# Kernel tuning notes

Measured on AMD Instinct MI355X. Metric: run time of the kernel, lower is better.

## Reference

```python
import jax, jax.numpy as jnp
import numpy as np

D = 2048      # d_hidden
F = 1408      # d_expert (routed)
E = 8         # n_routed_experts
K = 2         # n_experts_per_token
FS = 2816     # shared expert width = d_expert * n_shared_experts
B, S = 2, 1024


def setup_inputs() -> dict:
    key = jax.random.key(0)
    ks = jax.random.split(key, 9)
    sc = 0.02
    return {
        "x": jax.random.normal(ks[0], (B, S, D), dtype=jnp.float32),
        "Wr": jax.random.normal(ks[1], (E, D), dtype=jnp.float32) * sc,   # router Linear(d_hidden, E).weight
        "Wg": jax.random.normal(ks[2], (E, F, D), dtype=jnp.float32) * sc,  # per-expert W_gate.weight [F,D]
        "Wu": jax.random.normal(ks[3], (E, F, D), dtype=jnp.float32) * sc,  # per-expert W_up.weight
        "Wd": jax.random.normal(ks[4], (E, D, F), dtype=jnp.float32) * sc,  # per-expert W_down.weight [D,F]
        "Wsg": jax.random.normal(ks[5], (FS, D), dtype=jnp.float32) * sc,   # shared expert W_gate
        "Wsu": jax.random.normal(ks[6], (FS, D), dtype=jnp.float32) * sc,   # shared expert W_up
        "Wsd": jax.random.normal(ks[7], (D, FS), dtype=jnp.float32) * sc,   # shared expert W_down
    }


def reference(x, Wr, Wg, Wu, Wd, Wsg, Wsu, Wsd):
    silu = jax.nn.silu

    # Shared expert: SwiGLU FFN over all tokens
    sg = silu(jnp.einsum("bsd,fd->bsf", x, Wsg))
    su = jnp.einsum("bsd,fd->bsf", x, Wsu)
    shared_out = jnp.einsum("bsf,df->bsd", sg * su, Wsd)

    # Gating: softmax over expert logits, then top-k (sum-combine is order-invariant)
    logits = jnp.einsum("bsd,ed->bse", x, Wr)
    scores = jax.nn.softmax(logits, axis=-1)
    topk_scores, topk_idx = jax.lax.top_k(scores, K)            # [B,S,K]
    # Dense combine weights [B,S,E]: topk score where selected, else 0
    w_full = jnp.sum(jax.nn.one_hot(topk_idx, E, dtype=x.dtype) * topk_scores[..., None], axis=-2)

    # Routed experts (dense-over-experts equivalent of sorted grouped-GEMM dispatch)
    g = silu(jnp.einsum("bsd,efd->bsef", x, Wg))                # [B,S,E,F]
    u = jnp.einsum("bsd,efd->bsef", x, Wu)
    out_e = jnp.einsum("bsef,edf->bsed", g * u, Wd)             # [B,S,E,D]
    routed_out = jnp.einsum("bsed,bse->bsd", out_e, w_full)

    return routed_out + shared_out
```

## Files before the change

### kernel.cpp

```cpp
#include <hip/hip_runtime.h>
#include <hip/hip_bf16.h>

#define D_HID 2048
#define F_EXP 1408
#define E_NUM 8
#define FS_SH 2816
#define T_TOK 2048

#define O_WSG 0
#define O_WSU 5767168
#define O_WG  11534336
#define O_WU  34603008
#define O_WSD 57671680
#define O_WD  63438848
#define W_TOT 86507520

#define MAXT 24
#define GU_SH_BLK 176
#define GU_GEMM   440
#define GU_CONV   64
#define DN_GRID   512
#define DN_SH_BLK 128
#define RT_BLK    512
#define WC_BLK    1408

typedef __attribute__((ext_vector_type(8))) short bf16x8;
typedef __attribute__((ext_vector_type(4))) float f32x4;
typedef __attribute__((ext_vector_type(4))) unsigned short u16x4;

#define AS1 __attribute__((address_space(1)))
#define AS3 __attribute__((address_space(3)))

__device__ __forceinline__ unsigned short f2bf(float f){
  unsigned u = __float_as_uint(f);
  u += 0x7fffu + ((u >> 16) & 1u);
  return (unsigned short)(u >> 16);
}

__global__ __launch_bounds__(256) void prep_kernel(
    const float* __restrict__ x,  const float* __restrict__ Wr,
    const float* __restrict__ Wsg, const float* __restrict__ Wsu,
    const float* __restrict__ Wg,  const float* __restrict__ Wu,
    unsigned short* __restrict__ xb, unsigned short* __restrict__ wb,
    int* __restrict__ topk_e, float* __restrict__ topk_w)
{
  const int b = blockIdx.x;
  if (b >= RT_BLK){
    const int cb = b - RT_BLK;
    const long nchunk = (long)O_WSD / 8;
    for (long i = (long)cb*256 + threadIdx.x; i < nchunk; i += (long)WC_BLK*256){
      const long e0 = i * 8;
      const float* src; long lo;
      if      (e0 < (long)O_WSU){ src = Wsg; lo = e0; }
      else if (e0 < (long)O_WG ){ src = Wsu; lo = e0 - O_WSU; }
      else if (e0 < (long)O_WU ){ src = Wg;  lo = e0 - O_WG;  }
      else                      { src = Wu;  lo = e0 - O_WU;  }
      const float4 va = ((const float4*)(src + lo))[0];
      const float4 vb = ((const float4*)(src + lo))[1];
      u16x4 h0, h1;
      h0[0]=f2bf(va.x); h0[1]=f2bf(va.y); h0[2]=f2bf(va.z); h0[3]=f2bf(va.w);
      h1[0]=f2bf(vb.x); h1[1]=f2bf(vb.y); h1[2]=f2bf(vb.z); h1[3]=f2bf(vb.w);
      ((u16x4*)(wb + e0))[0] = h0;
      ((u16x4*)(wb + e0))[1] = h1;
    }
    return;
  }
  const int lane = threadIdx.x & 63;
  const int t = b*4 + (threadIdx.x >> 6);
  const float* xt = x + (size_t)t * D_HID;
  unsigned short* xbt = xb + (size_t)t * D_HID;
  float acc[E_NUM];
  #pragma unroll
  for (int e=0;e<E_NUM;e++) acc[e]=0.f;
  #pragma unroll
  for (int j=0;j<8;j++){
    const int d = j*256 + lane*4;
    const float4 v = *(const float4*)(xt + d);
    u16x4 h;
    h[0]=f2bf(v.x); h[1]=f2bf(v.y); h[2]=f2bf(v.z); h[3]=f2bf(v.w);
    *(u16x4*)(xbt + d) = h;
    #pragma unroll
    for (int e=0;e<E_NUM;e++){
      const float4 w = *(const float4*)(Wr + e*D_HID + d);
      acc[e] += v.x*w.x + v.y*w.y + v.z*w.z + v.w*w.w;
    }
  }
  #pragma unroll
  for (int e=0;e<E_NUM;e++){
    #pragma unroll
    for (int off=32; off>0; off>>=1) acc[e] += __shfl_xor(acc[e], off);
  }
  if (lane==0){
    float m = acc[0];
    #pragma unroll
    for (int e=1;e<E_NUM;e++) m = fmaxf(m, acc[e]);
    float p[E_NUM]; float s = 0.f;
    #pragma unroll
    for (int e=0;e<E_NUM;e++){ p[e] = expf(acc[e]-m); s += p[e]; }
    const float inv = 1.f/s;
    int i0=0; float b0=p[0];
    #pragma unroll
    for (int e=1;e<E_NUM;e++) if (p[e] > b0){ b0=p[e]; i0=e; }
    int i1=-1; float b1=-1.f;
    #pragma unroll
    for (int e=0;e<E_NUM;e++) if (e!=i0 && p[e] > b1){ b1=p[e]; i1=e; }
    topk_e[t*2+0]=i0; topk_e[t*2+1]=i1;
    topk_w[t*2+0]=b0*inv; topk_w[t*2+1]=b1*inv;
  }
}

__global__ __launch_bounds__(1024) void build_lists_kernel(
    const int* __restrict__ topk_e, const float* __restrict__ topk_w,
    int* __restrict__ cnt, int* __restrict__ offs,
    int* __restrict__ assign_token, float* __restrict__ assign_w,
    int* __restrict__ token_slot,
    int* __restrict__ tile_rowbase, int* __restrict__ tile_e,
    int* __restrict__ tile_valid, int* __restrict__ n_rt)
{
  const int tid  = threadIdx.x;
  const int lane = tid & 63;
  const int wv   = tid >> 6;
  __shared__ int wsum[E_NUM][16];
  __shared__ int tot_s[E_NUM];
  __shared__ int offs_s[E_NUM];

  int   e_loc[4];
  float w_loc[4];
  #pragma unroll
  for (int j=0;j<4;j++){ e_loc[j]=topk_e[tid*4+j]; w_loc[j]=topk_w[tid*4+j]; }

  int c[E_NUM];
  #pragma unroll
  for (int e=0;e<E_NUM;e++){
    int s = 0;
    #pragma unroll
    for (int j=0;j<4;j++) s += (e_loc[j]==e) ? 1 : 0;
    c[e] = s;
  }
  int pre[E_NUM];
  #pragma unroll
  for (int e=0;e<E_NUM;e++){
    int v = c[e];
    #pragma unroll
    for (int off=1; off<64; off<<=1){
      int t = __shfl_up(v, off);
      if (lane >= off) v += t;
    }
    if (lane==63) wsum[e][wv] = v;
    pre[e] = v - c[e];
  }
  __syncthreads();
  if (tid < E_NUM){
    int s = 0;
    #pragma unroll
    for (int w=0; w<16; w++){ int t = wsum[tid][w]; wsum[tid][w] = s; s += t; }
    tot_s[tid] = s;
    cnt[tid]   = s;
  }
  __syncthreads();
  if (tid == 0){
    int s = 0;
    #pragma unroll
    for (int e=0;e<E_NUM;e++){ offs_s[e] = s; offs[e] = s; s += tot_s[e]; }
    int ntl = 0;
    for (int e=0;e<E_NUM;e++){
      for (int r=0; r<tot_s[e]; r+=256){
        tile_rowbase[ntl] = offs_s[e] + r;
        tile_e[ntl]       = e;
        int v = tot_s[e] - r; if (v > 256) v = 256;
        tile_valid[ntl]   = v;
        ntl++;
      }
    }
    n_rt[0] = ntl;
    for (int i=ntl;i<MAXT;i++){ tile_rowbase[i]=0; tile_e[i]=0; tile_valid[i]=0; }
  }
  __syncthreads();
  int local[E_NUM];
  #pragma unroll
  for (int e=0;e<E_NUM;e++) local[e]=0;
  #pragma unroll
  for (int j=0;j<4;j++){
    const int e = e_loc[j];
    int pos = 0;
    #pragma unroll
    for (int ee=0; ee<E_NUM; ee++)
      if (e == ee) pos = offs_s[ee] + wsum[ee][wv] + pre[ee] + local[ee];
    #pragma unroll
    for (int ee=0; ee<E_NUM; ee++) local[ee] += (e == ee) ? 1 : 0;
    const int entry = tid*4 + j;
    assign_token[pos] = entry >> 1;
    assign_w[pos]     = w_loc[j];
    token_slot[entry] = pos;
  }
}

__global__ __launch_bounds__(512,1) void gateup_fused(
    const unsigned short* __restrict__ xb,
    unsigned short* __restrict__ wb,
    const float* __restrict__ Wsd_f, const float* __restrict__ Wd_f,
    unsigned short* __restrict__ h_shared,
    unsigned short* __restrict__ h_routed,
    const int* __restrict__ tile_rowbase, const int* __restrict__ tile_e,
    const int* __restrict__ tile_valid, const int* __restrict__ n_rt,
    const int* __restrict__ assign_token)
{
  __shared__ __align__(16) char As[4][256*64];
  __shared__ __align__(16) char Bg[4][128*64];
  __shared__ __align__(16) char Bu[4][128*64];

  const int tid  = threadIdx.x;
  const int braw = blockIdx.x;

  if (braw >= GU_GEMM){
    const int cb = braw - GU_GEMM;
    const long nchunk = (long)(W_TOT - O_WSD) / 8;
    for (long i = (long)cb*512 + tid; i < nchunk; i += (long)GU_CONV*512){
      const long e0 = (long)O_WSD + i * 8;
      const float* src; long lo;
      if (e0 < (long)O_WD){ src = Wsd_f; lo = e0 - O_WSD; } else { src = Wd_f; lo = e0 - O_WD; }
      const float4 va = ((const float4*)(src + lo))[0];
      const float4 vb = ((const float4*)(src + lo))[1];
      u16x4 h0, h1;
      h0[0]=f2bf(va.x); h0[1]=f2bf(va.y); h0[2]=f2bf(va.z); h0[3]=f2bf(va.w);
      h1[0]=f2bf(vb.x); h1[1]=f2bf(vb.y); h1[2]=f2bf(vb.z); h1[3]=f2bf(vb.w);
      ((u16x4*)(wb + e0))[0] = h0;
      ((u16x4*)(wb + e0))[1] = h1;
    }
    return;
  }

  const int b = (braw % 8) * (GU_GEMM/8) + braw / 8;

  const int lane = tid & 63;
  const int wave = tid >> 6;
  const int wr = wave >> 1;
  const int wc = wave & 1;

  int nt, rowbase, valid, gather;
  const unsigned short *wg_base, *wu_base;
  unsigned short* H; int N;
  if (b < GU_SH_BLK){
    nt = b >> 3; const int mtile = b & 7;
    rowbase = mtile*256; valid = 256; gather = 0;
    wg_base = wb + O_WSG + (size_t)(nt*128) * D_HID;
    wu_base = wb + O_WSU + (size_t)(nt*128) * D_HID;
    H = h_shared; N = FS_SH;
  } else {
    const int rb = b - GU_SH_BLK;
    const int tile = rb % MAXT;
    nt = rb / MAXT;
    if (tile >= n_rt[0]) return;
    rowbase = tile_rowbase[tile];
    valid   = tile_valid[tile];
    const int e = tile_e[tile];
    gather = 1;
    wg_base = wb + O_WG + ((size_t)e*F_EXP + nt*128) * D_HID;
    wu_base = wb + O_WU + ((size_t)e*F_EXP + nt*128) * D_HID;
    H = h_routed; N = F_EXP;
  }

  f32x4 accg[4][4], accu[4][4];
  const f32x4 z = {0.f,0.f,0.f,0.f};
  #pragma unroll
  for (int m=0;m<4;m++)
    #pragma unroll
    for (int n=0;n<4;n++){ accg[m][n]=z; accu[m][n]=z; }

  const char* asrc[2];
  const int rowmax = rowbase + valid - 1;
  #pragma unroll
  for (int p=0;p<2;p++){
    const int c = p*512 + tid;
    const int row = c >> 2, slot = c & 3;
    const int col16 = slot ^ ((row>>1)&3);
    int idx = rowbase + row;
    if (idx > rowmax) idx = rowmax;
    const size_t grow = gather ? (size_t)assign_token[idx] : (size_t)idx;
    asrc[p] = (const char*)(xb + grow * (size_t)D_HID) + (col16<<4);
  }
  const int brw = tid >> 2, bsl = tid & 3;
  const int bcol16 = bsl ^ ((brw>>1)&3);
  const char* gsrc = (const char*)(wg_base + (size_t)brw * D_HID) + (bcol16<<4);
  const char* usrc = (const char*)(wu_base + (size_t)brw * D_HID) + (bcol16<<4);

  auto stage = [&](int bi, int kt){
    #pragma unroll
    for (int p=0;p<2;p++)
      __builtin_amdgcn_global_load_lds(
        (const AS1 void*)(asrc[p] + kt*64),
        (AS3 void*)(&As[bi][(p*512 + tid)*16]), 16, 0, 0);
    __builtin_amdgcn_global_load_lds(
        (const AS1 void*)(gsrc + kt*64),
        (AS3 void*)(&Bg[bi][tid*16]), 16, 0, 0);
    __builtin_amdgcn_global_load_lds(
        (const AS1 void*)(usrc + kt*64),
        (AS3 void*)(&Bu[bi][tid*16]), 16, 0, 0);
  };

  const int nK = D_HID / 32;
  stage(0,0); stage(1,1); stage(2,2);

  const int arow0 = wr*64 + (lane & 15);
  const int brow0 = wc*64 + (lane & 15);
  const int sread = (lane >> 4) << 4;

  #pragma unroll 1
  for (int kt = 0; kt < nK; ++kt){
    if (kt < nK-2)       asm volatile("s_waitcnt vmcnt(8)\n\ts_barrier" ::: "memory");
    else if (kt == nK-2) asm volatile("s_waitcnt vmcnt(4)\n\ts_barrier" ::: "memory");
    else                 asm volatile("s_waitcnt vmcnt(0)\n\ts_barrier" ::: "memory");
    const int bi = kt & 3;
    bf16x8 a[4], bgr[4], bur[4];
    #pragma unroll
    for (int m=0;m<4;m++){
      const int r = arow0 + m*16;
      a[m] = *(const bf16x8*)(&As[bi][r*64 + (sread ^ (((r>>1)&3)<<4))]);
    }
    #pragma unroll
    for (int n=0;n<4;n++){
      const int r = brow0 + n*16;
      const int ofs = r*64 + (sread ^ (((r>>1)&3)<<4));
      bgr[n] = *(const bf16x8*)(&Bg[bi][ofs]);
      bur[n] = *(const bf16x8*)(&Bu[bi][ofs]);
    }
    if (kt + 3 < nK) stage((kt+3)&3, kt+3);
    #pragma unroll
    for (int m=0;m<4;m++)
      #pragma unroll
      for (int n=0;n<4;n++){
        accg[m][n] = __builtin_amdgcn_mfma_f32_16x16x32_bf16(a[m], bgr[n], accg[m][n], 0,0,0);
        accu[m][n] = __builtin_amdgcn_mfma_f32_16x16x32_bf16(a[m], bur[n], accu[m][n], 0,0,0);
      }
  }

  const int colbase = nt*128 + wc*64;
  #pragma unroll
  for (int m=0;m<4;m++){
    #pragma unroll
    for (int r=0;r<4;r++){
      const int rr = wr*64 + m*16 + ((lane >> 4) << 2) + r;
      if (rr < valid){
        unsigned short* orow = H + (size_t)(rowbase + rr) * N;
        #pragma unroll
        for (int n=0;n<4;n++){
          const int col = colbase + n*16 + (lane & 15);
          const float g = accg[m][n][r];
          const float u = accu[m][n][r];
          const float h = (g / (1.f + __expf(-g))) * u;
          orow[col] = f2bf(h);
        }
      }
    }
  }
}

__global__ __launch_bounds__(512,1) void down_fused(
    const unsigned short* __restrict__ h_shared,
    const unsigned short* __restrict__ h_routed,
    const unsigned short* __restrict__ wb,
    float* __restrict__ out, float* __restrict__ y_routed,
    const int* __restrict__ tile_rowbase, const int* __restrict__ tile_e,
    const int* __restrict__ tile_valid, const int* __restrict__ n_rt,
    const float* __restrict__ assign_w)
{
  __shared__ __align__(16) char As[4][256*64];
  __shared__ __align__(16) char Bs[4][128*64];

  const int tid  = threadIdx.x;
  const int braw = blockIdx.x;
  const int b = (braw % 8) * (DN_GRID/8) + braw / 8;
  const int lane = tid & 63;
  const int wave = tid >> 6;
  const int wr = wave >> 1, wc = wave & 1;

  int nt, rowbase, valid, weighted, K;
  const unsigned short *A, *w_base;
  float* Out;
  if (b < DN_SH_BLK){
    nt = b >> 3; const int mtile = b & 7;
    rowbase = mtile*256; valid = 256; weighted = 0;
    A = h_shared; K = FS_SH;
    w_base = wb + O_WSD + (size_t)(nt*128) * FS_SH;
    Out = out;
  } else {
    const int rb = b - DN_SH_BLK;
    const int tile = rb % MAXT;
    nt = rb / MAXT;
    if (tile >= n_rt[0]) return;
    rowbase = tile_rowbase[tile];
    valid   = tile_valid[tile];
    const int e = tile_e[tile];
    weighted = 1;
    A = h_routed; K = F_EXP;
    w_base = wb + O_WD + ((size_t)e*D_HID + nt*128) * F_EXP;
    Out = y_routed;
  }
  const size_t K2 = (size_t)K * 2;

  f32x4 acc[4][4];
  const f32x4 z = {0.f,0.f,0.f,0.f};
  #pragma unroll
  for (int m=0;m<4;m++)
    #pragma unroll
    for (int n=0;n<4;n++) acc[m][n]=z;

  const char* asrc[2];
  const int rowmax = rowbase + valid - 1;
  #pragma unroll
  for (int p=0;p<2;p++){
    const int c = p*512 + tid;
    const int row = c >> 2, slot = c & 3;
    const int col16 = slot ^ ((row>>1)&3);
    int idx = rowbase + row;
    if (idx > rowmax) idx = rowmax;
    asrc[p] = (const char*)A + (size_t)idx * K2 + (col16<<4);
  }
  const int brw = tid >> 2, bsl = tid & 3;
  const int bcol16 = bsl ^ ((brw>>1)&3);
  const char* bsrc = (const char*)w_base + (size_t)brw * K2 + (bcol16<<4);

  auto stage = [&](int bi, int kt){
    #pragma unroll
    for (int p=0;p<2;p++)
      __builtin_amdgcn_global_load_lds(
        (const AS1 void*)(asrc[p] + kt*64),
        (AS3 void*)(&As[bi][(p*512 + tid)*16]), 16, 0, 0);
    __builtin_amdgcn_global_load_lds(
        (const AS1 void*)(bsrc + kt*64),
        (AS3 void*)(&Bs[bi][tid*16]), 16, 0, 0);
  };

  const int nK = K / 32;
  stage(0,0); stage(1,1); stage(2,2);

  const int arow0 = wr*64 + (lane & 15);
  const int brow0 = wc*64 + (lane & 15);
  const int sread = (lane >> 4) << 4;

  #pragma unroll 1
  for (int kt = 0; kt < nK; ++kt){
    if (kt < nK-2)       asm volatile("s_waitcnt vmcnt(6)\n\ts_barrier" ::: "memory");
    else if (kt == nK-2) asm volatile("s_waitcnt vmcnt(3)\n\ts_barrier" ::: "memory");
    else                 asm volatile("s_waitcnt vmcnt(0)\n\ts_barrier" ::: "memory");
    const int bi = kt & 3;
    bf16x8 a[4], bb[4];
    #pragma unroll
    for (int m=0;m<4;m++){
      const int r = arow0 + m*16;
      a[m] = *(const bf16x8*)(&As[bi][r*64 + (sread ^ (((r>>1)&3)<<4))]);
    }
    #pragma unroll
    for (int n=0;n<4;n++){
      const int r = brow0 + n*16;
      bb[n] = *(const bf16x8*)(&Bs[bi][r*64 + (sread ^ (((r>>1)&3)<<4))]);
    }
    if (kt + 3 < nK) stage((kt+3)&3, kt+3);
    #pragma unroll
    for (int m=0;m<4;m++)
      #pragma unroll
      for (int n=0;n<4;n++)
        acc[m][n] = __builtin_amdgcn_mfma_f32_16x16x32_bf16(a[m], bb[n], acc[m][n], 0,0,0);
  }

  const int colbase = nt*128 + wc*64;
  #pragma unroll
  for (int m=0;m<4;m++){
    #pragma unroll
    for (int r=0;r<4;r++){
      const int rr = wr*64 + m*16 + ((lane >> 4) << 2) + r;
      if (rr < valid){
        float w = 1.f;
        if (weighted) w = assign_w[rowbase + rr];
        float* orow = Out + (size_t)(rowbase + rr) * D_HID;
        #pragma unroll
        for (int n=0;n<4;n++){
          const int col = colbase + n*16 + (lane & 15);
          orow[col] = acc[m][n][r] * w;
        }
      }
    }
  }
}

__global__ void combine_kernel(float* __restrict__ out, const float* __restrict__ y,
                               const int* __restrict__ token_slot){
  const int i  = blockIdx.x * blockDim.x + threadIdx.x;
  const int t  = i >> 9;
  const int r4 = i & 511;
  const int s0 = token_slot[t*2+0];
  const int s1 = token_slot[t*2+1];
  const float4 a = ((const float4*)(y + (size_t)s0 * D_HID))[r4];
  const float4 b = ((const float4*)(y + (size_t)s1 * D_HID))[r4];
  float4 o = ((float4*)out)[i];
  o.x += a.x + b.x; o.y += a.y + b.y; o.z += a.z + b.z; o.w += a.w + b.w;
  ((float4*)out)[i] = o;
}

extern "C" void kernel_launch(void* const* d_in, const int* in_sizes, int n_in,
                              void* d_out, int out_size, void* d_ws, size_t ws_size,
                              hipStream_t stream){
  const float* x   = (const float*)d_in[0];
  const float* Wr  = (const float*)d_in[1];
  const float* Wg  = (const float*)d_in[2];
  const float* Wu  = (const float*)d_in[3];
  const float* Wd  = (const float*)d_in[4];
  const float* Wsg = (const float*)d_in[5];
  const float* Wsu = (const float*)d_in[6];
  const float* Wsd = (const float*)d_in[7];
  float* out = (float*)d_out;
  (void)in_sizes; (void)n_in; (void)out_size; (void)ws_size;

  char* ws = (char*)d_ws;
  size_t off = 0;
  auto alloc = [&](size_t bytes)->char*{
    char* p = ws + off; off += (bytes + 255) & ~(size_t)255; return p;
  };

  unsigned short* wb       = (unsigned short*)alloc((size_t)W_TOT * 2);
  unsigned short* xb       = (unsigned short*)alloc((size_t)T_TOK * D_HID * 2);
  unsigned short* h_shared = (unsigned short*)alloc((size_t)T_TOK * FS_SH * 2);
  unsigned short* h_routed = (unsigned short*)alloc((size_t)T_TOK * 2 * F_EXP * 2);
  float*          y_routed = (float*)alloc((size_t)T_TOK * 2 * D_HID * 4);
  int*   topk_e       = (int*)alloc(T_TOK*2*sizeof(int));
  float* topk_w       = (float*)alloc(T_TOK*2*sizeof(float));
  int*   cnt          = (int*)alloc(E_NUM*sizeof(int));
  int*   offs         = (int*)alloc(E_NUM*sizeof(int));
  int*   assign_token = (int*)alloc(T_TOK*2*sizeof(int));
  float* assign_w     = (float*)alloc(T_TOK*2*sizeof(float));
  int*   token_slot   = (int*)alloc(T_TOK*2*sizeof(int));
  int*   tile_rowbase = (int*)alloc(MAXT*sizeof(int));
  int*   tile_e       = (int*)alloc(MAXT*sizeof(int));
  int*   tile_valid   = (int*)alloc(MAXT*sizeof(int));
  int*   n_rt         = (int*)alloc(sizeof(int));

  prep_kernel<<<RT_BLK + WC_BLK, 256, 0, stream>>>(
      x, Wr, Wsg, Wsu, Wg, Wu, xb, wb, topk_e, topk_w);
  build_lists_kernel<<<1, 1024, 0, stream>>>(topk_e, topk_w, cnt, offs,
      assign_token, assign_w, token_slot, tile_rowbase, tile_e, tile_valid, n_rt);

  gateup_fused<<<GU_GEMM + GU_CONV, 512, 0, stream>>>(
      xb, wb, Wsd, Wd, h_shared, h_routed, tile_rowbase, tile_e, tile_valid, n_rt, assign_token);
  down_fused<<<DN_GRID, 512, 0, stream>>>(
      h_shared, h_routed, wb, out, y_routed, tile_rowbase, tile_e, tile_valid, n_rt, assign_w);

  combine_kernel<<<(T_TOK*D_HID/4)/256, 256, 0, stream>>>(out, y_routed, token_slot);
}
```

Before: 371.9 us.

## Double-buffer LDS fragment reads in registers and raise MFMA wave priority

Both GEMM main loops are restructured so the A/B fragments for step kt+1 are read from LDS into a second register set while step kt's MFMAs run. The gate/up MFMAs are split into two passes, and MFMA sections are wrapped in s_setprio with one combined waitcnt and barrier per step. This aims to hide LDS read latency behind matrix math. Launch bounds also change to 2 blocks per CU. That caps registers and, given the large LDS footprint, may not raise occupancy and could cause spills.

```diff
diff --git a/kernel.cpp b/kernel.cpp
--- a/kernel.cpp
+++ b/kernel.cpp
@@ -195,7 +195,7 @@
   }
 }
 
-__global__ __launch_bounds__(512,1) void gateup_fused(
+__global__ __launch_bounds__(512,2) void gateup_fused(
     const unsigned short* __restrict__ xb,
     unsigned short* __restrict__ wb,
     const float* __restrict__ Wsd_f, const float* __restrict__ Wd_f,
@@ -298,20 +298,11 @@
         (AS3 void*)(&Bu[bi][tid*16]), 16, 0, 0);
   };
 
-  const int nK = D_HID / 32;
-  stage(0,0); stage(1,1); stage(2,2);
-
   const int arow0 = wr*64 + (lane & 15);
   const int brow0 = wc*64 + (lane & 15);
   const int sread = (lane >> 4) << 4;
 
-  #pragma unroll 1
-  for (int kt = 0; kt < nK; ++kt){
-    if (kt < nK-2)       asm volatile("s_waitcnt vmcnt(8)\n\ts_barrier" ::: "memory");
-    else if (kt == nK-2) asm volatile("s_waitcnt vmcnt(4)\n\ts_barrier" ::: "memory");
-    else                 asm volatile("s_waitcnt vmcnt(0)\n\ts_barrier" ::: "memory");
-    const int bi = kt & 3;
-    bf16x8 a[4], bgr[4], bur[4];
+  auto read_abg = [&](int bi, bf16x8* a, bf16x8* bg){
     #pragma unroll
     for (int m=0;m<4;m++){
       const int r = arow0 + m*16;
@@ -320,18 +311,51 @@
     #pragma unroll
     for (int n=0;n<4;n++){
       const int r = brow0 + n*16;
-      const int ofs = r*64 + (sread ^ (((r>>1)&3)<<4));
-      bgr[n] = *(const bf16x8*)(&Bg[bi][ofs]);
-      bur[n] = *(const bf16x8*)(&Bu[bi][ofs]);
+      bg[n] = *(const bf16x8*)(&Bg[bi][r*64 + (sread ^ (((r>>1)&3)<<4))]);
+    }
+  };
+
+  const int nK = D_HID / 32;
+  stage(0,0); stage(1,1); stage(2,2);
+  asm volatile("s_waitcnt vmcnt(8)\n\ts_barrier" ::: "memory");
+
+  bf16x8 aA[4], bgA[4], aB[4], bgB[4];
+  read_abg(0, aA, bgA);
+  asm volatile("s_waitcnt lgkmcnt(0) vmcnt(4)\n\ts_barrier" ::: "memory");
+
+  auto body = [&](int kt, bf16x8* aC, bf16x8* bgC, bf16x8* aN, bf16x8* bgN){
+    if (kt + 1 < nK) read_abg((kt+1)&3, aN, bgN);
+    bf16x8 bu[4];
+    {
+      const int bi = kt & 3;
+      #pragma unroll
+      for (int n=0;n<4;n++){
+        const int r = brow0 + n*16;
+        bu[n] = *(const bf16x8*)(&Bu[bi][r*64 + (sread ^ (((r>>1)&3)<<4))]);
+      }
     }
     if (kt + 3 < nK) stage((kt+3)&3, kt+3);
+    __builtin_amdgcn_s_setprio(1);
     #pragma unroll
     for (int m=0;m<4;m++)
       #pragma unroll
-      for (int n=0;n<4;n++){
-        accg[m][n] = __builtin_amdgcn_mfma_f32_16x16x32_bf16(a[m], bgr[n], accg[m][n], 0,0,0);
-        accu[m][n] = __builtin_amdgcn_mfma_f32_16x16x32_bf16(a[m], bur[n], accu[m][n], 0,0,0);
-      }
+      for (int n=0;n<4;n++)
+        accg[m][n] = __builtin_amdgcn_mfma_f32_16x16x32_bf16(aC[m], bgC[n], accg[m][n], 0,0,0);
+    #pragma unroll
+    for (int m=0;m<4;m++)
+      #pragma unroll
+      for (int n=0;n<4;n++)
+        accu[m][n] = __builtin_amdgcn_mfma_f32_16x16x32_bf16(aC[m], bu[n], accu[m][n], 0,0,0);
+    __builtin_amdgcn_s_setprio(0);
+    if (kt + 3 < nK) asm volatile("s_waitcnt lgkmcnt(0) vmcnt(4)\n\ts_barrier" ::: "memory");
+    else             asm volatile("s_waitcnt lgkmcnt(0) vmcnt(0)\n\ts_barrier" ::: "memory");
+    __builtin_amdgcn_sched_barrier(0);
+  };
+
+  #pragma unroll 1
+  for (int kt = 0; kt < nK; kt += 2){
+    body(kt,   aA, bgA, aB, bgB);
+    body(kt+1, aB, bgB, aA, bgA);
   }
 
   const int colbase = nt*128 + wc*64;
@@ -355,7 +379,7 @@
   }
 }
 
-__global__ __launch_bounds__(512,1) void down_fused(
+__global__ __launch_bounds__(512,2) void down_fused(
     const unsigned short* __restrict__ h_shared,
     const unsigned short* __restrict__ h_routed,
     const unsigned short* __restrict__ wb,
@@ -431,20 +455,11 @@
         (AS3 void*)(&Bs[bi][tid*16]), 16, 0, 0);
   };
 
-  const int nK = K / 32;
-  stage(0,0); stage(1,1); stage(2,2);
-
   const int arow0 = wr*64 + (lane & 15);
   const int brow0 = wc*64 + (lane & 15);
   const int sread = (lane >> 4) << 4;
 
-  #pragma unroll 1
-  for (int kt = 0; kt < nK; ++kt){
-    if (kt < nK-2)       asm volatile("s_waitcnt vmcnt(6)\n\ts_barrier" ::: "memory");
-    else if (kt == nK-2) asm volatile("s_waitcnt vmcnt(3)\n\ts_barrier" ::: "memory");
-    else                 asm volatile("s_waitcnt vmcnt(0)\n\ts_barrier" ::: "memory");
-    const int bi = kt & 3;
-    bf16x8 a[4], bb[4];
+  auto read_ab = [&](int bi, bf16x8* a, bf16x8* bb){
     #pragma unroll
     for (int m=0;m<4;m++){
       const int r = arow0 + m*16;
@@ -455,12 +470,35 @@
       const int r = brow0 + n*16;
       bb[n] = *(const bf16x8*)(&Bs[bi][r*64 + (sread ^ (((r>>1)&3)<<4))]);
     }
+  };
+
+  const int nK = K / 32;
+  stage(0,0); stage(1,1); stage(2,2);
+  asm volatile("s_waitcnt vmcnt(6)\n\ts_barrier" ::: "memory");
+
+  bf16x8 aA[4], bbA[4], aB[4], bbB[4];
+  read_ab(0, aA, bbA);
+  asm volatile("s_waitcnt lgkmcnt(0) vmcnt(3)\n\ts_barrier" ::: "memory");
+
+  auto body = [&](int kt, bf16x8* aC, bf16x8* bC, bf16x8* aN, bf16x8* bN){
+    if (kt + 1 < nK) read_ab((kt+1)&3, aN, bN);
     if (kt + 3 < nK) stage((kt+3)&3, kt+3);
+    __builtin_amdgcn_s_setprio(1);
     #pragma unroll
     for (int m=0;m<4;m++)
       #pragma unroll
       for (int n=0;n<4;n++)
-        acc[m][n] = __builtin_amdgcn_mfma_f32_16x16x32_bf16(a[m], bb[n], acc[m][n], 0,0,0);
+        acc[m][n] = __builtin_amdgcn_mfma_f32_16x16x32_bf16(aC[m], bC[n], acc[m][n], 0,0,0);
+    __builtin_amdgcn_s_setprio(0);
+    if (kt + 3 < nK) asm volatile("s_waitcnt lgkmcnt(0) vmcnt(3)\n\ts_barrier" ::: "memory");
+    else             asm volatile("s_waitcnt lgkmcnt(0) vmcnt(0)\n\ts_barrier" ::: "memory");
+    __builtin_amdgcn_sched_barrier(0);
+  };
+
+  #pragma unroll 1
+  for (int kt = 0; kt < nK; kt += 2){
+    body(kt,   aA, bbA, aB, bbB);
+    body(kt+1, aB, bbB, aA, bbA);
   }
 
   const int colbase = nt*128 + wc*64;
```

Measured after the change: 377.0 us. About the same (+1.4%).

## Shrink GEMM tiles to 128x128 with 256-thread blocks and double buffering

Applied to the files above, without the earlier changes.

Both fused GEMM kernels move from 256x128 tiles with 512 threads and a 4-stage LDS pipeline to 128x128 tiles with 256 threads and a 2-stage double buffer, so more blocks fit per CU. Routed-expert tiles are cut to 128 rows, which reduces padding waste for unevenly sized expert groups, and the grids grow to match. The cost is lower reuse of each weight tile (weights are streamed once per 128 rows instead of 256), a shallower prefetch depth, and an extra barrier per k-step.

```diff
diff --git a/kernel.cpp b/kernel.cpp
--- a/kernel.cpp
+++ b/kernel.cpp
@@ -15,12 +15,12 @@
 #define O_WD  63438848
 #define W_TOT 86507520
 
-#define MAXT 24
-#define GU_SH_BLK 176
-#define GU_GEMM   440
+#define MAXT 40
+#define GU_SH_BLK 352
+#define GU_GEMM   792
 #define GU_CONV   64
-#define DN_GRID   512
-#define DN_SH_BLK 128
+#define DN_SH_BLK 256
+#define DN_GRID   896
 #define RT_BLK    512
 #define WC_BLK    1408
 
@@ -164,10 +164,10 @@
     for (int e=0;e<E_NUM;e++){ offs_s[e] = s; offs[e] = s; s += tot_s[e]; }
     int ntl = 0;
     for (int e=0;e<E_NUM;e++){
-      for (int r=0; r<tot_s[e]; r+=256){
+      for (int r=0; r<tot_s[e]; r+=128){
         tile_rowbase[ntl] = offs_s[e] + r;
         tile_e[ntl]       = e;
-        int v = tot_s[e] - r; if (v > 256) v = 256;
+        int v = tot_s[e] - r; if (v > 128) v = 128;
         tile_valid[ntl]   = v;
         ntl++;
       }
@@ -195,7 +195,7 @@
   }
 }
 
-__global__ __launch_bounds__(512,1) void gateup_fused(
+__global__ __launch_bounds__(256,2) void gateup_fused(
     const unsigned short* __restrict__ xb,
     unsigned short* __restrict__ wb,
     const float* __restrict__ Wsd_f, const float* __restrict__ Wd_f,
@@ -205,9 +205,9 @@
     const int* __restrict__ tile_valid, const int* __restrict__ n_rt,
     const int* __restrict__ assign_token)
 {
-  __shared__ __align__(16) char As[4][256*64];
-  __shared__ __align__(16) char Bg[4][128*64];
-  __shared__ __align__(16) char Bu[4][128*64];
+  __shared__ __align__(16) char As[2][128*64];
+  __shared__ __align__(16) char Bg[2][128*64];
+  __shared__ __align__(16) char Bu[2][128*64];
 
   const int tid  = threadIdx.x;
   const int braw = blockIdx.x;
@@ -215,7 +215,7 @@
   if (braw >= GU_GEMM){
     const int cb = braw - GU_GEMM;
     const long nchunk = (long)(W_TOT - O_WSD) / 8;
-    for (long i = (long)cb*512 + tid; i < nchunk; i += (long)GU_CONV*512){
+    for (long i = (long)cb*256 + tid; i < nchunk; i += (long)GU_CONV*256){
       const long e0 = (long)O_WSD + i * 8;
       const float* src; long lo;
       if (e0 < (long)O_WD){ src = Wsd_f; lo = e0 - O_WSD; } else { src = Wd_f; lo = e0 - O_WD; }
@@ -241,8 +241,8 @@
   const unsigned short *wg_base, *wu_base;
   unsigned short* H; int N;
   if (b < GU_SH_BLK){
-    nt = b >> 3; const int mtile = b & 7;
-    rowbase = mtile*256; valid = 256; gather = 0;
+    nt = b >> 4; const int mtile = b & 15;
+    rowbase = mtile*128; valid = 128; gather = 0;
     wg_base = wb + O_WSG + (size_t)(nt*128) * D_HID;
     wu_base = wb + O_WSU + (size_t)(nt*128) * D_HID;
     H = h_shared; N = FS_SH;
@@ -271,7 +271,7 @@
   const int rowmax = rowbase + valid - 1;
   #pragma unroll
   for (int p=0;p<2;p++){
-    const int c = p*512 + tid;
+    const int c = p*256 + tid;
     const int row = c >> 2, slot = c & 3;
     const int col16 = slot ^ ((row>>1)&3);
     int idx = rowbase + row;
@@ -283,48 +283,53 @@
   const int bcol16 = bsl ^ ((brw>>1)&3);
   const char* gsrc = (const char*)(wg_base + (size_t)brw * D_HID) + (bcol16<<4);
   const char* usrc = (const char*)(wu_base + (size_t)brw * D_HID) + (bcol16<<4);
+  const int pstrB = 64 * D_HID * 2;
 
   auto stage = [&](int bi, int kt){
     #pragma unroll
     for (int p=0;p<2;p++)
       __builtin_amdgcn_global_load_lds(
         (const AS1 void*)(asrc[p] + kt*64),
-        (AS3 void*)(&As[bi][(p*512 + tid)*16]), 16, 0, 0);
-    __builtin_amdgcn_global_load_lds(
-        (const AS1 void*)(gsrc + kt*64),
-        (AS3 void*)(&Bg[bi][tid*16]), 16, 0, 0);
-    __builtin_amdgcn_global_load_lds(
-        (const AS1 void*)(usrc + kt*64),
-        (AS3 void*)(&Bu[bi][tid*16]), 16, 0, 0);
+        (AS3 void*)(&As[bi][(p*256 + tid)*16]), 16, 0, 0);
+    #pragma unroll
+    for (int p=0;p<2;p++){
+      __builtin_amdgcn_global_load_lds(
+        (const AS1 void*)(gsrc + p*pstrB + kt*64),
+        (AS3 void*)(&Bg[bi][(p*256 + tid)*16]), 16, 0, 0);
+      __builtin_amdgcn_global_load_lds(
+        (const AS1 void*)(usrc + p*pstrB + kt*64),
+        (AS3 void*)(&Bu[bi][(p*256 + tid)*16]), 16, 0, 0);
+    }
   };
-
-  const int nK = D_HID / 32;
-  stage(0,0); stage(1,1); stage(2,2);
 
   const int arow0 = wr*64 + (lane & 15);
   const int brow0 = wc*64 + (lane & 15);
   const int sread = (lane >> 4) << 4;
 
+  const int nK = D_HID / 32;
+  stage(0, 0);
+  int cur = 0;
   #pragma unroll 1
   for (int kt = 0; kt < nK; ++kt){
-    if (kt < nK-2)       asm volatile("s_waitcnt vmcnt(8)\n\ts_barrier" ::: "memory");
-    else if (kt == nK-2) asm volatile("s_waitcnt vmcnt(4)\n\ts_barrier" ::: "memory");
-    else                 asm volatile("s_waitcnt vmcnt(0)\n\ts_barrier" ::: "memory");
-    const int bi = kt & 3;
+    if (kt + 1 < nK){
+      stage(cur^1, kt+1);
+      asm volatile("s_waitcnt vmcnt(6)\n\ts_barrier" ::: "memory");
+    } else {
+      asm volatile("s_waitcnt vmcnt(0)\n\ts_barrier" ::: "memory");
+    }
     bf16x8 a[4], bgr[4], bur[4];
     #pragma unroll
     for (int m=0;m<4;m++){
       const int r = arow0 + m*16;
-      a[m] = *(const bf16x8*)(&As[bi][r*64 + (sread ^ (((r>>1)&3)<<4))]);
+      a[m] = *(const bf16x8*)(&As[cur][r*64 + (sread ^ (((r>>1)&3)<<4))]);
     }
     #pragma unroll
     for (int n=0;n<4;n++){
       const int r = brow0 + n*16;
       const int ofs = r*64 + (sread ^ (((r>>1)&3)<<4));
-      bgr[n] = *(const bf16x8*)(&Bg[bi][ofs]);
-      bur[n] = *(const bf16x8*)(&Bu[bi][ofs]);
-    }
-    if (kt + 3 < nK) stage((kt+3)&3, kt+3);
+      bgr[n] = *(const bf16x8*)(&Bg[cur][ofs]);
+      bur[n] = *(const bf16x8*)(&Bu[cur][ofs]);
+    }
     #pragma unroll
     for (int m=0;m<4;m++)
       #pragma unroll
@@ -332,6 +337,8 @@
         accg[m][n] = __builtin_amdgcn_mfma_f32_16x16x32_bf16(a[m], bgr[n], accg[m][n], 0,0,0);
         accu[m][n] = __builtin_amdgcn_mfma_f32_16x16x32_bf16(a[m], bur[n], accu[m][n], 0,0,0);
       }
+    asm volatile("s_barrier" ::: "memory");
+    cur ^= 1;
   }
 
   const int colbase = nt*128 + wc*64;
@@ -355,7 +362,7 @@
   }
 }
 
-__global__ __launch_bounds__(512,1) void down_fused(
+__global__ __launch_bounds__(256,3) void down_fused(
     const unsigned short* __restrict__ h_shared,
     const unsigned short* __restrict__ h_routed,
     const unsigned short* __restrict__ wb,
@@ -364,8 +371,8 @@
     const int* __restrict__ tile_valid, const int* __restrict__ n_rt,
     const float* __restrict__ assign_w)
 {
-  __shared__ __align__(16) char As[4][256*64];
-  __shared__ __align__(16) char Bs[4][128*64];
+  __shared__ __align__(16) char As[2][128*64];
+  __shared__ __align__(16) char Bs[2][128*64];
 
   const int tid  = threadIdx.x;
   const int braw = blockIdx.x;
@@ -378,8 +385,8 @@
   const unsigned short *A, *w_base;
   float* Out;
   if (b < DN_SH_BLK){
-    nt = b >> 3; const int mtile = b & 7;
-    rowbase = mtile*256; valid = 256; weighted = 0;
+    nt = b >> 4; const int mtile = b & 15;
+    rowbase = mtile*128; valid = 128; weighted = 0;
     A = h_shared; K = FS_SH;
     w_base = wb + O_WSD + (size_t)(nt*128) * FS_SH;
     Out = out;
@@ -409,7 +416,7 @@
   const int rowmax = rowbase + valid - 1;
   #pragma unroll
   for (int p=0;p<2;p++){
-    const int c = p*512 + tid;
+    const int c = p*256 + tid;
     const int row = c >> 2, slot = c & 3;
     const int col16 = slot ^ ((row>>1)&3);
     int idx = rowbase + row;
@@ -419,48 +426,54 @@
   const int brw = tid >> 2, bsl = tid & 3;
   const int bcol16 = bsl ^ ((brw>>1)&3);
   const char* bsrc = (const char*)w_base + (size_t)brw * K2 + (bcol16<<4);
+  const size_t pstrB = 64 * K2;
 
   auto stage = [&](int bi, int kt){
     #pragma unroll
     for (int p=0;p<2;p++)
       __builtin_amdgcn_global_load_lds(
         (const AS1 void*)(asrc[p] + kt*64),
-        (AS3 void*)(&As[bi][(p*512 + tid)*16]), 16, 0, 0);
-    __builtin_amdgcn_global_load_lds(
-        (const AS1 void*)(bsrc + kt*64),
-        (AS3 void*)(&Bs[bi][tid*16]), 16, 0, 0);
+        (AS3 void*)(&As[bi][(p*256 + tid)*16]), 16, 0, 0);
+    #pragma unroll
+    for (int p=0;p<2;p++)
+      __builtin_amdgcn_global_load_lds(
+        (const AS1 void*)(bsrc + p*pstrB + kt*64),
+        (AS3 void*)(&Bs[bi][(p*256 + tid)*16]), 16, 0, 0);
   };
-
-  const int nK = K / 32;
-  stage(0,0); stage(1,1); stage(2,2);
 
   const int arow0 = wr*64 + (lane & 15);
   const int brow0 = wc*64 + (lane & 15);
   const int sread = (lane >> 4) << 4;
 
+  const int nK = K / 32;
+  stage(0, 0);
+  int cur = 0;
   #pragma unroll 1
   for (int kt = 0; kt < nK; ++kt){
-    if (kt < nK-2)       asm volatile("s_waitcnt vmcnt(6)\n\ts_barrier" ::: "memory");
-    else if (kt == nK-2) asm volatile("s_waitcnt vmcnt(3)\n\ts_barrier" ::: "memory");
-    else                 asm volatile("s_waitcnt vmcnt(0)\n\ts_barrier" ::: "memory");
-    const int bi = kt & 3;
+    if (kt + 1 < nK){
+      stage(cur^1, kt+1);
+      asm volatile("s_waitcnt vmcnt(4)\n\ts_barrier" ::: "memory");
+    } else {
+      asm volatile("s_waitcnt vmcnt(0)\n\ts_barrier" ::: "memory");
+    }
     bf16x8 a[4], bb[4];
     #pragma unroll
     for (int m=0;m<4;m++){
       const int r = arow0 + m*16;
-      a[m] = *(const bf16x8*)(&As[bi][r*64 + (sread ^ (((r>>1)&3)<<4))]);
+      a[m] = *(const bf16x8*)(&As[cur][r*64 + (sread ^ (((r>>1)&3)<<4))]);
     }
     #pragma unroll
     for (int n=0;n<4;n++){
       const int r = brow0 + n*16;
-      bb[n] = *(const bf16x8*)(&Bs[bi][r*64 + (sread ^ (((r>>1)&3)<<4))]);
-    }
-    if (kt + 3 < nK) stage((kt+3)&3, kt+3);
+      bb[n] = *(const bf16x8*)(&Bs[cur][r*64 + (sread ^ (((r>>1)&3)<<4))]);
+    }
     #pragma unroll
     for (int m=0;m<4;m++)
       #pragma unroll
       for (int n=0;n<4;n++)
         acc[m][n] = __builtin_amdgcn_mfma_f32_16x16x32_bf16(a[m], bb[n], acc[m][n], 0,0,0);
+    asm volatile("s_barrier" ::: "memory");
+    cur ^= 1;
   }
 
   const int colbase = nt*128 + wc*64;
@@ -539,9 +552,9 @@
   build_lists_kernel<<<1, 1024, 0, stream>>>(topk_e, topk_w, cnt, offs,
       assign_token, assign_w, token_slot, tile_rowbase, tile_e, tile_valid, n_rt);
 
-  gateup_fused<<<GU_GEMM + GU_CONV, 512, 0, stream>>>(
+  gateup_fused<<<GU_GEMM + GU_CONV, 256, 0, stream>>>(
       xb, wb, Wsd, Wd, h_shared, h_routed, tile_rowbase, tile_e, tile_valid, n_rt, assign_token);
-  down_fused<<<DN_GRID, 512, 0, stream>>>(
+  down_fused<<<DN_GRID, 256, 0, stream>>>(
       h_shared, h_routed, wb, out, y_routed, tile_rowbase, tile_e, tile_valid, n_rt, assign_w);
 
   combine_kernel<<<(T_TOK*D_HID/4)/256, 256, 0, stream>>>(out, y_routed, token_slot);
```

Result: slower. 442.3 us (+18.9%).

## Widen down-projection N tile to 256 and store routed outputs as bf16

Applied to the files above, without the earlier changes.

The down-projection kernel now computes 256 output columns per block instead of 128, which halves the grid and doubles the B tile and the accumulator count. The aim is to reuse each A tile across more columns and cut redundant activation loads. Routed expert outputs are written as bf16 rather than fp32, and the top-k weighting moves into the combine kernel, reducing intermediate memory traffic. The risks are extra register pressure (about 128 accumulator registers under a launch bound of two blocks, which can cause spills), fewer blocks to fill the CUs, and a small precision loss from storing the routed partial outputs in bf16.

```diff
diff --git a/kernel.cpp b/kernel.cpp
--- a/kernel.cpp
+++ b/kernel.cpp
@@ -19,8 +19,8 @@
 #define GU_SH_BLK 176
 #define GU_GEMM   440
 #define GU_CONV   64
-#define DN_GRID   512
-#define DN_SH_BLK 128
+#define DN_SH_BLK 64
+#define DN_GRID   256
 #define RT_BLK    512
 #define WC_BLK    1408
 
@@ -35,6 +35,9 @@
   unsigned u = __float_as_uint(f);
   u += 0x7fffu + ((u >> 16) & 1u);
   return (unsigned short)(u >> 16);
+}
+__device__ __forceinline__ float bf2f(unsigned short h){
+  return __uint_as_float(((unsigned)h) << 16);
 }
 
 __global__ __launch_bounds__(256) void prep_kernel(
@@ -355,17 +358,16 @@
   }
 }
 
-__global__ __launch_bounds__(512,1) void down_fused(
+__global__ __launch_bounds__(512,2) void down_fused(
     const unsigned short* __restrict__ h_shared,
     const unsigned short* __restrict__ h_routed,
     const unsigned short* __restrict__ wb,
-    float* __restrict__ out, float* __restrict__ y_routed,
+    float* __restrict__ out, unsigned short* __restrict__ y_routed,
     const int* __restrict__ tile_rowbase, const int* __restrict__ tile_e,
-    const int* __restrict__ tile_valid, const int* __restrict__ n_rt,
-    const float* __restrict__ assign_w)
+    const int* __restrict__ tile_valid, const int* __restrict__ n_rt)
 {
   __shared__ __align__(16) char As[4][256*64];
-  __shared__ __align__(16) char Bs[4][128*64];
+  __shared__ __align__(16) char Bs[4][256*64];
 
   const int tid  = threadIdx.x;
   const int braw = blockIdx.x;
@@ -374,15 +376,13 @@
   const int wave = tid >> 6;
   const int wr = wave >> 1, wc = wave & 1;
 
-  int nt, rowbase, valid, weighted, K;
+  int nt, rowbase, valid, routed, K;
   const unsigned short *A, *w_base;
-  float* Out;
   if (b < DN_SH_BLK){
     nt = b >> 3; const int mtile = b & 7;
-    rowbase = mtile*256; valid = 256; weighted = 0;
+    rowbase = mtile*256; valid = 256; routed = 0;
     A = h_shared; K = FS_SH;
-    w_base = wb + O_WSD + (size_t)(nt*128) * FS_SH;
-    Out = out;
+    w_base = wb + O_WSD + (size_t)(nt*256) * FS_SH;
   } else {
     const int rb = b - DN_SH_BLK;
     const int tile = rb % MAXT;
@@ -391,19 +391,18 @@
     rowbase = tile_rowbase[tile];
     valid   = tile_valid[tile];
     const int e = tile_e[tile];
-    weighted = 1;
+    routed = 1;
     A = h_routed; K = F_EXP;
-    w_base = wb + O_WD + ((size_t)e*D_HID + nt*128) * F_EXP;
-    Out = y_routed;
+    w_base = wb + O_WD + ((size_t)e*D_HID + nt*256) * F_EXP;
   }
   const size_t K2 = (size_t)K * 2;
 
-  f32x4 acc[4][4];
+  f32x4 acc[4][8];
   const f32x4 z = {0.f,0.f,0.f,0.f};
   #pragma unroll
   for (int m=0;m<4;m++)
     #pragma unroll
-    for (int n=0;n<4;n++) acc[m][n]=z;
+    for (int n=0;n<8;n++) acc[m][n]=z;
 
   const char* asrc[2];
   const int rowmax = rowbase + valid - 1;
@@ -416,9 +415,14 @@
     if (idx > rowmax) idx = rowmax;
     asrc[p] = (const char*)A + (size_t)idx * K2 + (col16<<4);
   }
-  const int brw = tid >> 2, bsl = tid & 3;
-  const int bcol16 = bsl ^ ((brw>>1)&3);
-  const char* bsrc = (const char*)w_base + (size_t)brw * K2 + (bcol16<<4);
+  const char* bsrc[2];
+  #pragma unroll
+  for (int p=0;p<2;p++){
+    const int c = p*512 + tid;
+    const int row = c >> 2, slot = c & 3;
+    const int col16 = slot ^ ((row>>1)&3);
+    bsrc[p] = (const char*)(w_base + (size_t)row * K) + (col16<<4);
+  }
 
   auto stage = [&](int bi, int kt){
     #pragma unroll
@@ -426,32 +430,34 @@
       __builtin_amdgcn_global_load_lds(
         (const AS1 void*)(asrc[p] + kt*64),
         (AS3 void*)(&As[bi][(p*512 + tid)*16]), 16, 0, 0);
-    __builtin_amdgcn_global_load_lds(
-        (const AS1 void*)(bsrc + kt*64),
-        (AS3 void*)(&Bs[bi][tid*16]), 16, 0, 0);
+    #pragma unroll
+    for (int p=0;p<2;p++)
+      __builtin_amdgcn_global_load_lds(
+        (const AS1 void*)(bsrc[p] + kt*64),
+        (AS3 void*)(&Bs[bi][(p*512 + tid)*16]), 16, 0, 0);
   };
 
   const int nK = K / 32;
   stage(0,0); stage(1,1); stage(2,2);
 
   const int arow0 = wr*64 + (lane & 15);
-  const int brow0 = wc*64 + (lane & 15);
+  const int brow0 = wc*128 + (lane & 15);
   const int sread = (lane >> 4) << 4;
 
   #pragma unroll 1
   for (int kt = 0; kt < nK; ++kt){
-    if (kt < nK-2)       asm volatile("s_waitcnt vmcnt(6)\n\ts_barrier" ::: "memory");
-    else if (kt == nK-2) asm volatile("s_waitcnt vmcnt(3)\n\ts_barrier" ::: "memory");
+    if (kt < nK-2)       asm volatile("s_waitcnt vmcnt(8)\n\ts_barrier" ::: "memory");
+    else if (kt == nK-2) asm volatile("s_waitcnt vmcnt(4)\n\ts_barrier" ::: "memory");
     else                 asm volatile("s_waitcnt vmcnt(0)\n\ts_barrier" ::: "memory");
     const int bi = kt & 3;
-    bf16x8 a[4], bb[4];
+    bf16x8 a[4], bb[8];
     #pragma unroll
     for (int m=0;m<4;m++){
       const int r = arow0 + m*16;
       a[m] = *(const bf16x8*)(&As[bi][r*64 + (sread ^ (((r>>1)&3)<<4))]);
     }
     #pragma unroll
-    for (int n=0;n<4;n++){
+    for (int n=0;n<8;n++){
       const int r = brow0 + n*16;
       bb[n] = *(const bf16x8*)(&Bs[bi][r*64 + (sread ^ (((r>>1)&3)<<4))]);
     }
@@ -459,41 +465,54 @@
     #pragma unroll
     for (int m=0;m<4;m++)
       #pragma unroll
-      for (int n=0;n<4;n++)
+      for (int n=0;n<8;n++)
         acc[m][n] = __builtin_amdgcn_mfma_f32_16x16x32_bf16(a[m], bb[n], acc[m][n], 0,0,0);
   }
 
-  const int colbase = nt*128 + wc*64;
+  const int colbase = nt*256 + wc*128;
   #pragma unroll
   for (int m=0;m<4;m++){
     #pragma unroll
     for (int r=0;r<4;r++){
       const int rr = wr*64 + m*16 + ((lane >> 4) << 2) + r;
       if (rr < valid){
-        float w = 1.f;
-        if (weighted) w = assign_w[rowbase + rr];
-        float* orow = Out + (size_t)(rowbase + rr) * D_HID;
-        #pragma unroll
-        for (int n=0;n<4;n++){
-          const int col = colbase + n*16 + (lane & 15);
-          orow[col] = acc[m][n][r] * w;
+        if (routed){
+          unsigned short* orow = y_routed + (size_t)(rowbase + rr) * D_HID;
+          #pragma unroll
+          for (int n=0;n<8;n++){
+            const int col = colbase + n*16 + (lane & 15);
+            orow[col] = f2bf(acc[m][n][r]);
+          }
+        } else {
+          float* orow = out + (size_t)(rowbase + rr) * D_HID;
+          #pragma unroll
+          for (int n=0;n<8;n++){
+            const int col = colbase + n*16 + (lane & 15);
+            orow[col] = acc[m][n][r];
+          }
         }
       }
     }
   }
 }
 
-__global__ void combine_kernel(float* __restrict__ out, const float* __restrict__ y,
-                               const int* __restrict__ token_slot){
+__global__ void combine_kernel(float* __restrict__ out, const unsigned short* __restrict__ y,
+                               const int* __restrict__ token_slot,
+                               const float* __restrict__ topk_w){
   const int i  = blockIdx.x * blockDim.x + threadIdx.x;
   const int t  = i >> 9;
   const int r4 = i & 511;
   const int s0 = token_slot[t*2+0];
   const int s1 = token_slot[t*2+1];
-  const float4 a = ((const float4*)(y + (size_t)s0 * D_HID))[r4];
-  const float4 b = ((const float4*)(y + (size_t)s1 * D_HID))[r4];
+  const float w0 = topk_w[t*2+0];
+  const float w1 = topk_w[t*2+1];
+  const u16x4 a = ((const u16x4*)(y + (size_t)s0 * D_HID))[r4];
+  const u16x4 bq = ((const u16x4*)(y + (size_t)s1 * D_HID))[r4];
   float4 o = ((float4*)out)[i];
-  o.x += a.x + b.x; o.y += a.y + b.y; o.z += a.z + b.z; o.w += a.w + b.w;
+  o.x += w0*bf2f(a[0]) + w1*bf2f(bq[0]);
+  o.y += w0*bf2f(a[1]) + w1*bf2f(bq[1]);
+  o.z += w0*bf2f(a[2]) + w1*bf2f(bq[2]);
+  o.w += w0*bf2f(a[3]) + w1*bf2f(bq[3]);
   ((float4*)out)[i] = o;
 }
 
@@ -521,7 +540,7 @@
   unsigned short* xb       = (unsigned short*)alloc((size_t)T_TOK * D_HID * 2);
   unsigned short* h_shared = (unsigned short*)alloc((size_t)T_TOK * FS_SH * 2);
   unsigned short* h_routed = (unsigned short*)alloc((size_t)T_TOK * 2 * F_EXP * 2);
-  float*          y_routed = (float*)alloc((size_t)T_TOK * 2 * D_HID * 4);
+  unsigned short* y_routed = (unsigned short*)alloc((size_t)T_TOK * 2 * D_HID * 2);
   int*   topk_e       = (int*)alloc(T_TOK*2*sizeof(int));
   float* topk_w       = (float*)alloc(T_TOK*2*sizeof(float));
   int*   cnt          = (int*)alloc(E_NUM*sizeof(int));
@@ -542,7 +561,7 @@
   gateup_fused<<<GU_GEMM + GU_CONV, 512, 0, stream>>>(
       xb, wb, Wsd, Wd, h_shared, h_routed, tile_rowbase, tile_e, tile_valid, n_rt, assign_token);
   down_fused<<<DN_GRID, 512, 0, stream>>>(
-      h_shared, h_routed, wb, out, y_routed, tile_rowbase, tile_e, tile_valid, n_rt, assign_w);
-
-  combine_kernel<<<(T_TOK*D_HID/4)/256, 256, 0, stream>>>(out, y_routed, token_slot);
-}
+      h_shared, h_routed, wb, out, y_routed, tile_rowbase, tile_e, tile_valid, n_rt);
+
+  combine_kernel<<<(T_TOK*D_HID/4)/256, 256, 0, stream>>>(out, y_routed, token_slot, topk_w);
+}
```

Result: faster. 333.3 us (-10.4%).
